# Optimization experiments

Measured on AMD Instinct MI355X. Metric: run time of the kernel, lower is better.

The kernel has to match this reference:

```python
import jax, jax.numpy as jnp
import numpy as np

N_NODES = 50000
N_EDGES = 600000
N_GRAPHS = 64
IN_D, HID, EMB = 5, 128, 64
BN_EPS = 1e-5


def setup_inputs() -> dict:
    key = jax.random.key(0)
    ks = jax.random.split(key, 16)
    x = jax.random.normal(ks[0], (N_NODES, IN_D), dtype=jnp.float32)
    src = jax.random.randint(ks[1], (N_EDGES,), 0, N_NODES, dtype=jnp.int32)
    dst = jax.random.randint(ks[2], (N_EDGES,), 0, N_NODES, dtype=jnp.int32)
    batch = jnp.sort(jax.random.randint(ks[3], (N_NODES,), 0, N_GRAPHS, dtype=jnp.int32))
    def lin(k, fi, fo):
        s = 1.0 / np.sqrt(fi)
        kw, kb = jax.random.split(k)
        return (jax.random.uniform(kw, (fi, fo), jnp.float32, -s, s),
                jax.random.uniform(kb, (fo,), jnp.float32, -s, s))
    W1, b1 = lin(ks[4], IN_D, HID)
    W2, b2 = lin(ks[5], HID, HID)
    W3, b3 = lin(ks[6], HID, HID)
    Wp, bp = lin(ks[7], HID, EMB)
    g1 = 1.0 + 0.1 * jax.random.normal(ks[8], (HID,), jnp.float32)
    g2 = 1.0 + 0.1 * jax.random.normal(ks[9], (HID,), jnp.float32)
    g3 = 1.0 + 0.1 * jax.random.normal(ks[10], (HID,), jnp.float32)
    be1 = 0.1 * jax.random.normal(ks[11], (HID,), jnp.float32)
    be2 = 0.1 * jax.random.normal(ks[12], (HID,), jnp.float32)
    be3 = 0.1 * jax.random.normal(ks[13], (HID,), jnp.float32)
    return dict(x=x, src=src, dst=dst, batch=batch,
                W1=W1, b1=b1, W2=W2, b2=b2, W3=W3, b3=b3,
                g1=g1, be1=be1, g2=g2, be2=be2, g3=g3, be3=be3,
                Wp=Wp, bp=bp)


def reference(x, src, dst, batch, W1, b1, W2, b2, W3, b3,
              g1, be1, g2, be2, g3, be3, Wp, bp):
    n = x.shape[0]
    # GCNConv with self-loops and symmetric normalization (PyG default)
    loop = jnp.arange(n, dtype=src.dtype)
    s = jnp.concatenate([src, loop])
    d = jnp.concatenate([dst, loop])
    deg = jax.ops.segment_sum(jnp.ones_like(d, dtype=x.dtype), d, num_segments=n)
    dinv = jnp.where(deg > 0, jax.lax.rsqrt(deg), 0.0)
    norm = (dinv[s] * dinv[d])[:, None]  # (E+N, 1)

    def gcn(h, W, b):
        hw = h @ W                                   # (N, HID)
        msg = hw[s] * norm                           # gather + scale
        agg = jax.ops.segment_sum(msg, d, num_segments=n)
        return agg + b

    def bn_relu(h, g, be):
        # eval-mode BatchNorm1d with running_mean=0, running_var=1
        return jax.nn.relu(h * (g * jax.lax.rsqrt(jnp.asarray(1.0 + BN_EPS, h.dtype))) + be)

    h = bn_relu(gcn(x, W1, b1), g1, be1)
    h = bn_relu(gcn(h, W2, b2), g2, be2)
    h = bn_relu(gcn(h, W3, b3), g3, be3)

    # global mean pool over graphs
    sums = jax.ops.segment_sum(h, batch, num_segments=N_GRAPHS)
    cnt = jax.ops.segment_sum(jnp.ones((n,), h.dtype), batch, num_segments=N_GRAPHS)
    pooled = sums / jnp.maximum(cnt, 1.0)[:, None]
    return pooled @ Wp + bp
```

## Files before the change

kernel.cpp:

```cpp
#include <hip/hip_runtime.h>
#include <hip/hip_fp16.h>

#define N_NODES 50000
#define N_EDGES 600000
#define N_GRAPHS 64
#define IN_D 5
#define HID 128
#define EMB 64

#define CHUNK 512
#define NCHUNK ((N_NODES + CHUNK - 1) / CHUNK)
#define NREP 16
#define NLOC 4
#define TB 16

typedef _Float16 half8 __attribute__((ext_vector_type(8)));
typedef float float4v __attribute__((ext_vector_type(4)));
typedef float floatx2 __attribute__((ext_vector_type(2)));

__device__ __forceinline__ float ep_w(unsigned pe) {
    return (float)__ushort_as_half((unsigned short)(pe >> 16));
}
__device__ __forceinline__ unsigned ep_s(unsigned pe) { return pe & 0xffffu; }


__global__ __launch_bounds__(256) void k_init(
        int* __restrict__ cnt, float* __restrict__ psum_rep,
        const float* __restrict__ W2, const float* __restrict__ W3,
        _Float16* __restrict__ Wt2, _Float16* __restrict__ Wt3,
        unsigned int* __restrict__ e_pack,
        const float* __restrict__ x, float* __restrict__ xp) {
    int tid = blockIdx.x * blockDim.x + threadIdx.x;
    int nt = gridDim.x * blockDim.x;
    for (int i = tid; i < N_NODES; i += nt) cnt[i] = 0;
    for (int i = tid; i < NREP * N_GRAPHS * HID; i += nt) psum_rep[i] = 0.f;
    if (tid < 8) e_pack[N_EDGES + tid] = 0u;
    for (int i = tid; i < N_NODES * 8; i += nt) {
        int f = i & 7, n = i >> 3;
        xp[i] = (f < IN_D) ? x[n * IN_D + f] : 0.f;
    }
    for (int i = tid; i < 2 * HID * HID; i += nt) {
        int rem = i & (HID * HID - 1);
        int k = rem & 127, f = rem >> 7;
        if (i < HID * HID) Wt2[rem] = (_Float16)W2[k * HID + f];
        else               Wt3[rem] = (_Float16)W3[k * HID + f];
    }
}


__global__ __launch_bounds__(256) void k_count(
        const int* __restrict__ dst, int* __restrict__ cnt) {
    int e = blockIdx.x * blockDim.x + threadIdx.x;
    if (e < N_EDGES) atomicAdd(&cnt[dst[e]], 1);
}


__global__ void k_chunksum(const int* __restrict__ cnt, int* __restrict__ csum,
                           float* __restrict__ dinv) {
    __shared__ int sh[256];
    int b = blockIdx.x, t = threadIdx.x;
    int i0 = b * CHUNK + t, i1 = i0 + 256;
    int v = 0;
    if (i0 < N_NODES) { int c = cnt[i0]; v += c; dinv[i0] = rsqrtf((float)c + 1.0f); }
    if (i1 < N_NODES) { int c = cnt[i1]; v += c; dinv[i1] = rsqrtf((float)c + 1.0f); }
    sh[t] = v; __syncthreads();
    for (int off = 128; off > 0; off >>= 1) {
        if (t < off) sh[t] += sh[t + off];
        __syncthreads();
    }
    if (t == 0) csum[b] = sh[0];
}


__global__ void k_scan(const int* __restrict__ cnt, const int* __restrict__ csum,
                       int* __restrict__ row_start) {
    __shared__ int ws[4];
    int b = blockIdx.x, t = threadIdx.x;
    int lane = t & 63, w = t >> 6;

    int pre = 0;
    for (int j = lane; j < b; j += 64) pre += csum[j];
    #pragma unroll
    for (int off = 32; off > 0; off >>= 1) pre += __shfl_down(pre, off);
    pre = __shfl(pre, 0);

    int base = b * CHUNK;
    int i0 = base + 2 * t, i1 = i0 + 1;
    int c0 = (i0 < N_NODES) ? cnt[i0] : 0;
    int c1 = (i1 < N_NODES) ? cnt[i1] : 0;
    int v = c0 + c1;
    int s = v;
    #pragma unroll
    for (int off = 1; off < 64; off <<= 1) {
        int u = __shfl_up(s, off);
        if (lane >= off) s += u;
    }
    if (lane == 63) ws[w] = s;
    __syncthreads();
    if (t == 0) {
        int r = 0;
        #pragma unroll
        for (int j = 0; j < 4; ++j) { int xx = ws[j]; ws[j] = r; r += xx; }
    }
    __syncthreads();
    int excl = s - v + ws[w] + pre;
    if (i0 < N_NODES) row_start[i0] = excl;
    if (i1 < N_NODES) row_start[i1] = excl + c0;
    if (b == 0 && t == 0) row_start[N_NODES] = N_EDGES;
}


__global__ __launch_bounds__(256) void k_scatter(
        const int* __restrict__ src, const int* __restrict__ dst,
        const float* __restrict__ dinv, const int* __restrict__ row_start,
        int* __restrict__ cnt, unsigned int* __restrict__ e_pack) {
    int e = blockIdx.x * blockDim.x + threadIdx.x;
    if (e >= N_EDGES) return;
    int d = dst[e];
    int pos = row_start[d] + atomicSub(&cnt[d], 1) - 1;
    int s = src[e];
    unsigned hw = (unsigned)__half_as_ushort(__float2half(dinv[s]));
    e_pack[pos] = (hw << 16) | (unsigned)s;
}


__global__ __launch_bounds__(256) void k_agg1(
        const float* __restrict__ xp, const float* __restrict__ dinv,
        const int* __restrict__ row_start, const unsigned int* __restrict__ e_pack,
        const float* __restrict__ W1, const float* __restrict__ b1,
        const float* __restrict__ g1, const float* __restrict__ be1,
        unsigned short* __restrict__ H8u) {
    int t = threadIdx.x;
    int w = t >> 6, lane = t & 63;
    int slot8 = lane >> 3, q8 = lane & 7;
    int nb = blockIdx.x * TB;

    const float rs = rsqrtf(1.0f + 1e-5f);
    int fa = lane * 2, fb = fa + 1;
    float w1a[IN_D], w1b[IN_D];
    #pragma unroll
    for (int k = 0; k < IN_D; ++k) {
        w1a[k] = W1[k * HID + fa];
        w1b[k] = W1[k * HID + fb];
    }
    float b1a = b1[fa], b1b = b1[fb];
    float g1a = g1[fa] * rs, g1b = g1[fb] * rs;
    float e1a = be1[fa], e1b = be1[fb];

    #pragma unroll 1
    for (int i = 0; i < 4; ++i) {
        int n = nb + w * 4 + i;
        int beg = row_start[n], end = row_start[n + 1];
        float acc = 0.f;
        for (int e = beg; e < end; e += 8) {
            unsigned pe = e_pack[e + slot8];
            float fw = (e + slot8 < end) ? ep_w(pe) : 0.f;
            float g = xp[(size_t)ep_s(pe) * 8 + q8];
            acc = fmaf(fw, g, acc);
        }
        acc += __shfl_xor(acc, 8);
        acc += __shfl_xor(acc, 16);
        acc += __shfl_xor(acc, 32);
        float di = dinv[n];
        float av = di * fmaf(di, xp[(size_t)n * 8 + q8], acc);
        float a0 = __shfl(av, 0), a1 = __shfl(av, 1), a2 = __shfl(av, 2),
              a3 = __shfl(av, 3), a4 = __shfl(av, 4);
        float va = b1a, vb = b1b;
        va = fmaf(a0, w1a[0], va); vb = fmaf(a0, w1b[0], vb);
        va = fmaf(a1, w1a[1], va); vb = fmaf(a1, w1b[1], vb);
        va = fmaf(a2, w1a[2], va); vb = fmaf(a2, w1b[2], vb);
        va = fmaf(a3, w1a[3], va); vb = fmaf(a3, w1b[3], vb);
        va = fmaf(a4, w1a[4], va); vb = fmaf(a4, w1b[4], vb);
        va = fmaf(va, g1a, e1a);
        vb = fmaf(vb, g1b, e1b);
        va = va > 0.f ? va : 0.f;
        vb = vb > 0.f ? vb : 0.f;
        int p = __builtin_amdgcn_cvt_pk_fp8_f32(va, vb, 0, false);
        H8u[(size_t)n * 64 + lane] = (unsigned short)(p & 0xffff);
    }
}


__device__ __forceinline__ void agg_node_fp8(
        const unsigned int* __restrict__ H8, const float* __restrict__ dinv,
        const int* __restrict__ row_start, const unsigned int* __restrict__ e_pack,
        int n, int slot8, int q8, _Float16* __restrict__ asrow) {
    float acc[16];
    #pragma unroll
    for (int j = 0; j < 16; ++j) acc[j] = 0.f;
    int beg = row_start[n], end = row_start[n + 1];
    for (int e = beg; e < end; e += 8) {
        unsigned pe = e_pack[e + slot8];
        float fw = (e + slot8 < end) ? ep_w(pe) : 0.f;
        uint4 g = ((const uint4*)(H8 + (size_t)ep_s(pe) * 32))[q8];
        unsigned int gw[4] = {g.x, g.y, g.z, g.w};
        #pragma unroll
        for (int q = 0; q < 4; ++q) {
            floatx2 lo = __builtin_amdgcn_cvt_pk_f32_fp8(gw[q], false);
            floatx2 hi = __builtin_amdgcn_cvt_pk_f32_fp8(gw[q], true);
            acc[4 * q + 0] = fmaf(fw, lo[0], acc[4 * q + 0]);
            acc[4 * q + 1] = fmaf(fw, lo[1], acc[4 * q + 1]);
            acc[4 * q + 2] = fmaf(fw, hi[0], acc[4 * q + 2]);
            acc[4 * q + 3] = fmaf(fw, hi[1], acc[4 * q + 3]);
        }
    }
    #pragma unroll
    for (int j = 0; j < 16; ++j) {
        float a = acc[j];
        a += __shfl_xor(a, 8);
        a += __shfl_xor(a, 16);
        a += __shfl_xor(a, 32);
        acc[j] = a;
    }
    if (slot8 == 0) {
        float di = dinv[n];
        uint4 s = ((const uint4*)(H8 + (size_t)n * 32))[q8];
        unsigned int sw[4] = {s.x, s.y, s.z, s.w};
        float sv[16];
        #pragma unroll
        for (int q = 0; q < 4; ++q) {
            floatx2 lo = __builtin_amdgcn_cvt_pk_f32_fp8(sw[q], false);
            floatx2 hi = __builtin_amdgcn_cvt_pk_f32_fp8(sw[q], true);
            sv[4 * q + 0] = lo[0]; sv[4 * q + 1] = lo[1];
            sv[4 * q + 2] = hi[0]; sv[4 * q + 3] = hi[1];
        }
        half8 o0, o1;
        #pragma unroll
        for (int j = 0; j < 8; ++j)
            o0[j] = (_Float16)(di * fmaf(di, sv[j], acc[j]));
        #pragma unroll
        for (int j = 0; j < 8; ++j)
            o1[j] = (_Float16)(di * fmaf(di, sv[j + 8], acc[j + 8]));
        *(half8*)(asrow + q8 * 16) = o0;
        *(half8*)(asrow + q8 * 16 + 8) = o1;
    }
}


__global__ __launch_bounds__(256) void k_fuse2(
        const unsigned int* __restrict__ Hin, const float* __restrict__ dinv,
        const int* __restrict__ row_start, const unsigned int* __restrict__ e_pack,
        const _Float16* __restrict__ Wt,
        const float* __restrict__ bb, const float* __restrict__ gg,
        const float* __restrict__ bee, unsigned char* __restrict__ out8) {
    __shared__ __align__(16) _Float16 As[TB][136];
    int t = threadIdx.x;
    int w = t >> 6, lane = t & 63;
    int slot8 = lane >> 3, q8 = lane & 7;
    int nb = blockIdx.x * TB;

    #pragma unroll 1
    for (int i = 0; i < 4; ++i)
        agg_node_fp8(Hin, dinv, row_start, e_pack,
                     nb + w * 4 + i, slot8, q8, &As[w * 4 + i][0]);
    __syncthreads();

    int quad = lane >> 4, r16 = lane & 15;
    half8 a[4];
    #pragma unroll
    for (int kb = 0; kb < 4; ++kb)
        a[kb] = *(const half8*)&As[r16][(kb * 4 + quad) * 8];
    const float rs = rsqrtf(1.0f + 1e-5f);
    #pragma unroll
    for (int fi = 0; fi < 2; ++fi) {
        int f = (w * 2 + fi) * 16 + r16;
        const half8* Brow = (const half8*)(Wt + (size_t)f * 128);
        float4v acc = {0.f, 0.f, 0.f, 0.f};
        #pragma unroll
        for (int kb = 0; kb < 4; ++kb)
            acc = __builtin_amdgcn_mfma_f32_16x16x32_f16(a[kb], Brow[kb * 4 + quad],
                                                         acc, 0, 0, 0);
        float b0 = bb[f], gf = gg[f] * rs, e0 = bee[f];
        #pragma unroll
        for (int rr = 0; rr < 4; ++rr) {
            float v = fmaf(acc[rr] + b0, gf, e0);
            v = v > 0.f ? v : 0.f;
            int p = __builtin_amdgcn_cvt_pk_fp8_f32(v, 0.f, 0, false);
            out8[(size_t)(nb + quad * 4 + rr) * 128 + f] = (unsigned char)(p & 0xff);
        }
    }
}


__global__ __launch_bounds__(256) void k_fuse3(
        const unsigned int* __restrict__ Hin, const float* __restrict__ dinv,
        const int* __restrict__ row_start, const unsigned int* __restrict__ e_pack,
        const _Float16* __restrict__ Wt,
        const float* __restrict__ bb, const float* __restrict__ gg,
        const float* __restrict__ bee, const int* __restrict__ batch,
        float* __restrict__ psum_rep) {
    __shared__ __align__(16) _Float16 As[TB][136];
    __shared__ float sh_pool[NLOC][HID];
    int t = threadIdx.x;
    int w = t >> 6, lane = t & 63;
    int slot8 = lane >> 3, q8 = lane & 7;
    int blk = (int)blockIdx.x;
    int nb = blk * TB;

    for (int i = t; i < NLOC * HID; i += 256) ((float*)sh_pool)[i] = 0.f;
    __syncthreads();

    #pragma unroll 1
    for (int i = 0; i < 4; ++i)
        agg_node_fp8(Hin, dinv, row_start, e_pack,
                     nb + w * 4 + i, slot8, q8, &As[w * 4 + i][0]);

    int quad = lane >> 4, r16 = lane & 15;
    int g0 = batch[nb];
    int gi4[4];
    #pragma unroll
    for (int rr = 0; rr < 4; ++rr) gi4[rr] = batch[nb + quad * 4 + rr];
    __syncthreads();

    half8 a[4];
    #pragma unroll
    for (int kb = 0; kb < 4; ++kb)
        a[kb] = *(const half8*)&As[r16][(kb * 4 + quad) * 8];
    float* rep = psum_rep + (size_t)(blk & (NREP - 1)) * N_GRAPHS * HID;
    const float rs = rsqrtf(1.0f + 1e-5f);
    #pragma unroll
    for (int fi = 0; fi < 2; ++fi) {
        int f = (w * 2 + fi) * 16 + r16;
        const half8* Brow = (const half8*)(Wt + (size_t)f * 128);
        float4v acc = {0.f, 0.f, 0.f, 0.f};
        #pragma unroll
        for (int kb = 0; kb < 4; ++kb)
            acc = __builtin_amdgcn_mfma_f32_16x16x32_f16(a[kb], Brow[kb * 4 + quad],
                                                         acc, 0, 0, 0);
        float b0 = bb[f], gf = gg[f] * rs, e0 = bee[f];
        float partial = 0.f;
        int cur = -1;
        #pragma unroll
        for (int rr = 0; rr < 4; ++rr) {
            float v = fmaf(acc[rr] + b0, gf, e0);
            v = v > 0.f ? v : 0.f;
            int gi = gi4[rr];
            if (gi != cur) {
                if (cur >= 0) {
                    int idx = cur - g0;
                    if (idx < NLOC) atomicAdd(&sh_pool[idx][f], partial);
                    else            atomicAdd(&rep[cur * HID + f], partial);
                }
                partial = 0.f; cur = gi;
            }
            partial += v;
        }
        if (cur >= 0) {
            int idx = cur - g0;
            if (idx < NLOC) atomicAdd(&sh_pool[idx][f], partial);
            else            atomicAdd(&rep[cur * HID + f], partial);
        }
    }
    __syncthreads();
    for (int i = t; i < NLOC * HID; i += 256) {
        int idx = i >> 7, ff = i & 127;
        float v = sh_pool[idx][ff];
        int g = g0 + idx;
        if (v != 0.f && g < N_GRAPHS) atomicAdd(&rep[g * HID + ff], v);
    }
}


__device__ __forceinline__ int lower_bound_batch(const int* __restrict__ batch, int val) {
    int lo = 0, hi = N_NODES;
    while (lo < hi) {
        int mid = (lo + hi) >> 1;
        if (batch[mid] < val) lo = mid + 1;
        else hi = mid;
    }
    return lo;
}

__global__ void k_final(const float* __restrict__ psum_rep, const int* __restrict__ batch,
                        const float* __restrict__ Wp, const float* __restrict__ bp,
                        float* __restrict__ out) {
    __shared__ float s_p[HID];
    int gi = blockIdx.x, e = threadIdx.x;
    for (int f = e; f < HID; f += EMB) {
        float v = 0.f;
        #pragma unroll
        for (int r = 0; r < NREP; ++r)
            v += psum_rep[(size_t)r * N_GRAPHS * HID + gi * HID + f];
        s_p[f] = v;
    }
    int lane = e & 63;
    int r = 0;
    if (lane < 2) r = lower_bound_batch(batch, gi + lane);
    int c0 = __shfl(r, 0), c1 = __shfl(r, 1);
    float inv = 1.0f / fmaxf((float)(c1 - c0), 1.0f);
    __syncthreads();
    float acc = bp[e];
    #pragma unroll 8
    for (int f = 0; f < HID; ++f)
        acc = fmaf(s_p[f] * inv, Wp[f * EMB + e], acc);
    out[gi * EMB + e] = acc;
}


extern "C" void kernel_launch(void* const* d_in, const int* in_sizes, int n_in,
                              void* d_out, int out_size, void* d_ws, size_t ws_size,
                              hipStream_t stream) {
    const float* x   = (const float*)d_in[0];
    const int*   src = (const int*)d_in[1];
    const int*   dst = (const int*)d_in[2];
    const int* batch = (const int*)d_in[3];
    const float* W1 = (const float*)d_in[4];
    const float* b1 = (const float*)d_in[5];
    const float* W2 = (const float*)d_in[6];
    const float* b2 = (const float*)d_in[7];
    const float* W3 = (const float*)d_in[8];
    const float* b3 = (const float*)d_in[9];
    const float* g1 = (const float*)d_in[10];
    const float* be1 = (const float*)d_in[11];
    const float* g2 = (const float*)d_in[12];
    const float* be2 = (const float*)d_in[13];
    const float* g3 = (const float*)d_in[14];
    const float* be3 = (const float*)d_in[15];
    const float* Wp = (const float*)d_in[16];
    const float* bp = (const float*)d_in[17];
    float* out = (float*)d_out;

    char* ws = (char*)d_ws;
    size_t o = 0;
    auto alloc = [&](size_t bytes) {
        void* pp = ws + o;
        o += bytes;
        o = (o + 255) & ~255ull;
        return pp;
    };
    int*      cnt       = (int*)alloc(N_NODES * 4);
    int*      row_start = (int*)alloc((N_NODES + 1) * 4);
    int*      csum      = (int*)alloc(NCHUNK * 4);
    float*    dinv      = (float*)alloc(N_NODES * 4);
    unsigned int* e_pack = (unsigned int*)alloc((size_t)(N_EDGES + 8) * 4);
    _Float16* Wt2       = (_Float16*)alloc(HID * HID * 2);
    _Float16* Wt3       = (_Float16*)alloc(HID * HID * 2);
    float*    xp        = (float*)alloc((size_t)N_NODES * 8 * 4);
    unsigned int* H8a   = (unsigned int*)alloc((size_t)N_NODES * HID);
    unsigned int* H8b   = (unsigned int*)alloc((size_t)N_NODES * HID);
    float*    psum_rep  = (float*)alloc((size_t)NREP * N_GRAPHS * HID * 4);

    k_init<<<512, 256, 0, stream>>>(cnt, psum_rep, W2, W3, Wt2, Wt3, e_pack, x, xp);
    k_count<<<(N_EDGES + 255) / 256, 256, 0, stream>>>(dst, cnt);
    k_chunksum<<<NCHUNK, 256, 0, stream>>>(cnt, csum, dinv);
    k_scan<<<NCHUNK, 256, 0, stream>>>(cnt, csum, row_start);
    k_scatter<<<(N_EDGES + 255) / 256, 256, 0, stream>>>(src, dst, dinv, row_start,
                                                         cnt, e_pack);
    k_agg1<<<N_NODES / TB, 256, 0, stream>>>(xp, dinv, row_start, e_pack,
                                             W1, b1, g1, be1, (unsigned short*)H8a);
    k_fuse2<<<N_NODES / TB, 256, 0, stream>>>(H8a, dinv, row_start, e_pack, Wt2,
                                              b2, g2, be2, (unsigned char*)H8b);
    k_fuse3<<<N_NODES / TB, 256, 0, stream>>>(H8b, dinv, row_start, e_pack, Wt3,
                                              b3, g3, be3, batch, psum_rep);
    k_final<<<N_GRAPHS, EMB, 0, stream>>>(psum_rep, batch, Wp, bp, out);
}
```

Before: 270.7 us.

## Interleave edge gathers for node pairs and fold setup work into count kernel

New measurement: 262.5 us. 3.0% less time.

```diff
diff --git a/kernel.cpp b/kernel.cpp
--- a/kernel.cpp
+++ b/kernel.cpp
@@ -24,17 +24,24 @@
 __device__ __forceinline__ unsigned ep_s(unsigned pe) { return pe & 0xffffu; }
 
 
-__global__ __launch_bounds__(256) void k_init(
-        int* __restrict__ cnt, float* __restrict__ psum_rep,
+__global__ __launch_bounds__(256) void k_init(int* __restrict__ cnt) {
+    int tid = blockIdx.x * blockDim.x + threadIdx.x;
+    if (tid < N_NODES) cnt[tid] = 0;
+}
+
+
+__global__ __launch_bounds__(256) void k_count(
+        const int* __restrict__ dst, int* __restrict__ cnt,
+        float* __restrict__ psum_rep,
         const float* __restrict__ W2, const float* __restrict__ W3,
         _Float16* __restrict__ Wt2, _Float16* __restrict__ Wt3,
         unsigned int* __restrict__ e_pack,
         const float* __restrict__ x, float* __restrict__ xp) {
     int tid = blockIdx.x * blockDim.x + threadIdx.x;
     int nt = gridDim.x * blockDim.x;
-    for (int i = tid; i < N_NODES; i += nt) cnt[i] = 0;
+    if (tid < N_EDGES) atomicAdd(&cnt[dst[tid]], 1);
+    if (tid < 8) e_pack[N_EDGES + tid] = 0u;
     for (int i = tid; i < NREP * N_GRAPHS * HID; i += nt) psum_rep[i] = 0.f;
-    if (tid < 8) e_pack[N_EDGES + tid] = 0u;
     for (int i = tid; i < N_NODES * 8; i += nt) {
         int f = i & 7, n = i >> 3;
         xp[i] = (f < IN_D) ? x[n * IN_D + f] : 0.f;
@@ -45,13 +52,6 @@
         if (i < HID * HID) Wt2[rem] = (_Float16)W2[k * HID + f];
         else               Wt3[rem] = (_Float16)W3[k * HID + f];
     }
-}
-
-
-__global__ __launch_bounds__(256) void k_count(
-        const int* __restrict__ dst, int* __restrict__ cnt) {
-    int e = blockIdx.x * blockDim.x + threadIdx.x;
-    if (e < N_EDGES) atomicAdd(&cnt[dst[e]], 1);
 }
 
 
@@ -148,91 +148,149 @@
     float e1a = be1[fa], e1b = be1[fb];
 
     #pragma unroll 1
-    for (int i = 0; i < 4; ++i) {
-        int n = nb + w * 4 + i;
-        int beg = row_start[n], end = row_start[n + 1];
-        float acc = 0.f;
-        for (int e = beg; e < end; e += 8) {
-            unsigned pe = e_pack[e + slot8];
-            float fw = (e + slot8 < end) ? ep_w(pe) : 0.f;
-            float g = xp[(size_t)ep_s(pe) * 8 + q8];
-            acc = fmaf(fw, g, acc);
-        }
-        acc += __shfl_xor(acc, 8);
-        acc += __shfl_xor(acc, 16);
-        acc += __shfl_xor(acc, 32);
-        float di = dinv[n];
-        float av = di * fmaf(di, xp[(size_t)n * 8 + q8], acc);
-        float a0 = __shfl(av, 0), a1 = __shfl(av, 1), a2 = __shfl(av, 2),
-              a3 = __shfl(av, 3), a4 = __shfl(av, 4);
-        float va = b1a, vb = b1b;
-        va = fmaf(a0, w1a[0], va); vb = fmaf(a0, w1b[0], vb);
-        va = fmaf(a1, w1a[1], va); vb = fmaf(a1, w1b[1], vb);
-        va = fmaf(a2, w1a[2], va); vb = fmaf(a2, w1b[2], vb);
-        va = fmaf(a3, w1a[3], va); vb = fmaf(a3, w1b[3], vb);
-        va = fmaf(a4, w1a[4], va); vb = fmaf(a4, w1b[4], vb);
-        va = fmaf(va, g1a, e1a);
-        vb = fmaf(vb, g1b, e1b);
-        va = va > 0.f ? va : 0.f;
-        vb = vb > 0.f ? vb : 0.f;
-        int p = __builtin_amdgcn_cvt_pk_fp8_f32(va, vb, 0, false);
-        H8u[(size_t)n * 64 + lane] = (unsigned short)(p & 0xffff);
-    }
-}
-
-
-__device__ __forceinline__ void agg_node_fp8(
+    for (int i = 0; i < 2; ++i) {
+        int n0 = nb + w * 4 + i * 2;
+        int beg0 = row_start[n0], end0 = row_start[n0 + 1], end1 = row_start[n0 + 2];
+        float acc0 = 0.f, acc1 = 0.f;
+        int e0 = beg0, e1 = end0;
+        while (e0 < end0 && e1 < end1) {
+            unsigned pe0 = e_pack[e0 + slot8];
+            unsigned pe1 = e_pack[e1 + slot8];
+            float fw0 = (e0 + slot8 < end0) ? ep_w(pe0) : 0.f;
+            float fw1 = (e1 + slot8 < end1) ? ep_w(pe1) : 0.f;
+            float v0 = xp[(size_t)ep_s(pe0) * 8 + q8];
+            float v1 = xp[(size_t)ep_s(pe1) * 8 + q8];
+            acc0 = fmaf(fw0, v0, acc0);
+            acc1 = fmaf(fw1, v1, acc1);
+            e0 += 8; e1 += 8;
+        }
+        while (e0 < end0) {
+            unsigned pe0 = e_pack[e0 + slot8];
+            float fw0 = (e0 + slot8 < end0) ? ep_w(pe0) : 0.f;
+            acc0 = fmaf(fw0, xp[(size_t)ep_s(pe0) * 8 + q8], acc0);
+            e0 += 8;
+        }
+        while (e1 < end1) {
+            unsigned pe1 = e_pack[e1 + slot8];
+            float fw1 = (e1 + slot8 < end1) ? ep_w(pe1) : 0.f;
+            acc1 = fmaf(fw1, xp[(size_t)ep_s(pe1) * 8 + q8], acc1);
+            e1 += 8;
+        }
+        #pragma unroll
+        for (int off = 8; off < 64; off <<= 1) {
+            acc0 += __shfl_xor(acc0, off);
+            acc1 += __shfl_xor(acc1, off);
+        }
+        #pragma unroll
+        for (int p2 = 0; p2 < 2; ++p2) {
+            int n = n0 + p2;
+            float accs = p2 ? acc1 : acc0;
+            float di = dinv[n];
+            float av = di * fmaf(di, xp[(size_t)n * 8 + q8], accs);
+            float a0 = __shfl(av, 0), a1 = __shfl(av, 1), a2 = __shfl(av, 2),
+                  a3 = __shfl(av, 3), a4 = __shfl(av, 4);
+            float va = b1a, vb = b1b;
+            va = fmaf(a0, w1a[0], va); vb = fmaf(a0, w1b[0], vb);
+            va = fmaf(a1, w1a[1], va); vb = fmaf(a1, w1b[1], vb);
+            va = fmaf(a2, w1a[2], va); vb = fmaf(a2, w1b[2], vb);
+            va = fmaf(a3, w1a[3], va); vb = fmaf(a3, w1b[3], vb);
+            va = fmaf(a4, w1a[4], va); vb = fmaf(a4, w1b[4], vb);
+            va = fmaf(va, g1a, e1a);
+            vb = fmaf(vb, g1b, e1b);
+            va = va > 0.f ? va : 0.f;
+            vb = vb > 0.f ? vb : 0.f;
+            int p = __builtin_amdgcn_cvt_pk_fp8_f32(va, vb, 0, false);
+            H8u[(size_t)n * 64 + lane] = (unsigned short)(p & 0xffff);
+        }
+    }
+}
+
+
+__device__ __forceinline__ void acc_row_fp8(float* __restrict__ acc, float fw, uint4 g) {
+    unsigned int gw[4] = {g.x, g.y, g.z, g.w};
+    #pragma unroll
+    for (int q = 0; q < 4; ++q) {
+        floatx2 lo = __builtin_amdgcn_cvt_pk_f32_fp8(gw[q], false);
+        floatx2 hi = __builtin_amdgcn_cvt_pk_f32_fp8(gw[q], true);
+        acc[4 * q + 0] = fmaf(fw, lo[0], acc[4 * q + 0]);
+        acc[4 * q + 1] = fmaf(fw, lo[1], acc[4 * q + 1]);
+        acc[4 * q + 2] = fmaf(fw, hi[0], acc[4 * q + 2]);
+        acc[4 * q + 3] = fmaf(fw, hi[1], acc[4 * q + 3]);
+    }
+}
+
+__device__ __forceinline__ void agg_pair_fp8(
         const unsigned int* __restrict__ H8, const float* __restrict__ dinv,
         const int* __restrict__ row_start, const unsigned int* __restrict__ e_pack,
-        int n, int slot8, int q8, _Float16* __restrict__ asrow) {
-    float acc[16];
-    #pragma unroll
-    for (int j = 0; j < 16; ++j) acc[j] = 0.f;
-    int beg = row_start[n], end = row_start[n + 1];
-    for (int e = beg; e < end; e += 8) {
-        unsigned pe = e_pack[e + slot8];
-        float fw = (e + slot8 < end) ? ep_w(pe) : 0.f;
-        uint4 g = ((const uint4*)(H8 + (size_t)ep_s(pe) * 32))[q8];
-        unsigned int gw[4] = {g.x, g.y, g.z, g.w};
+        int n0, int slot8, int q8,
+        _Float16* __restrict__ row0, _Float16* __restrict__ row1) {
+    float acc0[16], acc1[16];
+    #pragma unroll
+    for (int j = 0; j < 16; ++j) { acc0[j] = 0.f; acc1[j] = 0.f; }
+    int beg0 = row_start[n0], end0 = row_start[n0 + 1], end1 = row_start[n0 + 2];
+    int e0 = beg0, e1 = end0;
+    while (e0 < end0 && e1 < end1) {
+        unsigned pe0 = e_pack[e0 + slot8];
+        unsigned pe1 = e_pack[e1 + slot8];
+        float fw0 = (e0 + slot8 < end0) ? ep_w(pe0) : 0.f;
+        float fw1 = (e1 + slot8 < end1) ? ep_w(pe1) : 0.f;
+        uint4 g0 = ((const uint4*)(H8 + (size_t)ep_s(pe0) * 32))[q8];
+        uint4 g1 = ((const uint4*)(H8 + (size_t)ep_s(pe1) * 32))[q8];
+        acc_row_fp8(acc0, fw0, g0);
+        acc_row_fp8(acc1, fw1, g1);
+        e0 += 8; e1 += 8;
+    }
+    while (e0 < end0) {
+        unsigned pe0 = e_pack[e0 + slot8];
+        float fw0 = (e0 + slot8 < end0) ? ep_w(pe0) : 0.f;
+        uint4 g0 = ((const uint4*)(H8 + (size_t)ep_s(pe0) * 32))[q8];
+        acc_row_fp8(acc0, fw0, g0);
+        e0 += 8;
+    }
+    while (e1 < end1) {
+        unsigned pe1 = e_pack[e1 + slot8];
+        float fw1 = (e1 + slot8 < end1) ? ep_w(pe1) : 0.f;
+        uint4 g1 = ((const uint4*)(H8 + (size_t)ep_s(pe1) * 32))[q8];
+        acc_row_fp8(acc1, fw1, g1);
+        e1 += 8;
+    }
+    #pragma unroll
+    for (int j = 0; j < 16; ++j) {
+        float a = acc0[j];
+        a += __shfl_xor(a, 8); a += __shfl_xor(a, 16); a += __shfl_xor(a, 32);
+        acc0[j] = a;
+        float b = acc1[j];
+        b += __shfl_xor(b, 8); b += __shfl_xor(b, 16); b += __shfl_xor(b, 32);
+        acc1[j] = b;
+    }
+    if (slot8 == 0) {
+        float di0 = dinv[n0], di1 = dinv[n0 + 1];
+        uint4 s0 = ((const uint4*)(H8 + (size_t)n0 * 32))[q8];
+        uint4 s1 = ((const uint4*)(H8 + (size_t)(n0 + 1) * 32))[q8];
+        unsigned int sw0[4] = {s0.x, s0.y, s0.z, s0.w};
+        unsigned int sw1[4] = {s1.x, s1.y, s1.z, s1.w};
+        half8 o0a, o0b, o1a, o1b;
         #pragma unroll
         for (int q = 0; q < 4; ++q) {
-            floatx2 lo = __builtin_amdgcn_cvt_pk_f32_fp8(gw[q], false);
-            floatx2 hi = __builtin_amdgcn_cvt_pk_f32_fp8(gw[q], true);
-            acc[4 * q + 0] = fmaf(fw, lo[0], acc[4 * q + 0]);
-            acc[4 * q + 1] = fmaf(fw, lo[1], acc[4 * q + 1]);
-            acc[4 * q + 2] = fmaf(fw, hi[0], acc[4 * q + 2]);
-            acc[4 * q + 3] = fmaf(fw, hi[1], acc[4 * q + 3]);
-        }
-    }
-    #pragma unroll
-    for (int j = 0; j < 16; ++j) {
-        float a = acc[j];
-        a += __shfl_xor(a, 8);
-        a += __shfl_xor(a, 16);
-        a += __shfl_xor(a, 32);
-        acc[j] = a;
-    }
-    if (slot8 == 0) {
-        float di = dinv[n];
-        uint4 s = ((const uint4*)(H8 + (size_t)n * 32))[q8];
-        unsigned int sw[4] = {s.x, s.y, s.z, s.w};
-        float sv[16];
-        #pragma unroll
-        for (int q = 0; q < 4; ++q) {
-            floatx2 lo = __builtin_amdgcn_cvt_pk_f32_fp8(sw[q], false);
-            floatx2 hi = __builtin_amdgcn_cvt_pk_f32_fp8(sw[q], true);
-            sv[4 * q + 0] = lo[0]; sv[4 * q + 1] = lo[1];
-            sv[4 * q + 2] = hi[0]; sv[4 * q + 3] = hi[1];
-        }
-        half8 o0, o1;
-        #pragma unroll
-        for (int j = 0; j < 8; ++j)
-            o0[j] = (_Float16)(di * fmaf(di, sv[j], acc[j]));
-        #pragma unroll
-        for (int j = 0; j < 8; ++j)
-            o1[j] = (_Float16)(di * fmaf(di, sv[j + 8], acc[j + 8]));
-        *(half8*)(asrow + q8 * 16) = o0;
-        *(half8*)(asrow + q8 * 16 + 8) = o1;
+            floatx2 lo0 = __builtin_amdgcn_cvt_pk_f32_fp8(sw0[q], false);
+            floatx2 hi0 = __builtin_amdgcn_cvt_pk_f32_fp8(sw0[q], true);
+            floatx2 lo1 = __builtin_amdgcn_cvt_pk_f32_fp8(sw1[q], false);
+            floatx2 hi1 = __builtin_amdgcn_cvt_pk_f32_fp8(sw1[q], true);
+            int j = 4 * q;
+            float f0[4] = {lo0[0], lo0[1], hi0[0], hi0[1]};
+            float f1[4] = {lo1[0], lo1[1], hi1[0], hi1[1]};
+            #pragma unroll
+            for (int u = 0; u < 4; ++u) {
+                float r0 = di0 * fmaf(di0, f0[u], acc0[j + u]);
+                float r1 = di1 * fmaf(di1, f1[u], acc1[j + u]);
+                if (j + u < 8) { o0a[j + u] = (_Float16)r0; o1a[j + u] = (_Float16)r1; }
+                else           { o0b[j + u - 8] = (_Float16)r0; o1b[j + u - 8] = (_Float16)r1; }
+            }
+        }
+        *(half8*)(row0 + q8 * 16)     = o0a;
+        *(half8*)(row0 + q8 * 16 + 8) = o0b;
+        *(half8*)(row1 + q8 * 16)     = o1a;
+        *(half8*)(row1 + q8 * 16 + 8) = o1b;
     }
 }
 
@@ -250,9 +308,9 @@
     int nb = blockIdx.x * TB;
 
     #pragma unroll 1
-    for (int i = 0; i < 4; ++i)
-        agg_node_fp8(Hin, dinv, row_start, e_pack,
-                     nb + w * 4 + i, slot8, q8, &As[w * 4 + i][0]);
+    for (int i = 0; i < 2; ++i)
+        agg_pair_fp8(Hin, dinv, row_start, e_pack, nb + w * 4 + i * 2,
+                     slot8, q8, &As[w * 4 + i * 2][0], &As[w * 4 + i * 2 + 1][0]);
     __syncthreads();
 
     int quad = lane >> 4, r16 = lane & 15;
@@ -301,9 +359,9 @@
     __syncthreads();
 
     #pragma unroll 1
-    for (int i = 0; i < 4; ++i)
-        agg_node_fp8(Hin, dinv, row_start, e_pack,
-                     nb + w * 4 + i, slot8, q8, &As[w * 4 + i][0]);
+    for (int i = 0; i < 2; ++i)
+        agg_pair_fp8(Hin, dinv, row_start, e_pack, nb + w * 4 + i * 2,
+                     slot8, q8, &As[w * 4 + i * 2][0], &As[w * 4 + i * 2 + 1][0]);
 
     int quad = lane >> 4, r16 = lane & 15;
     int g0 = batch[nb];
@@ -440,8 +498,9 @@
     unsigned int* H8b   = (unsigned int*)alloc((size_t)N_NODES * HID);
     float*    psum_rep  = (float*)alloc((size_t)NREP * N_GRAPHS * HID * 4);
 
-    k_init<<<512, 256, 0, stream>>>(cnt, psum_rep, W2, W3, Wt2, Wt3, e_pack, x, xp);
-    k_count<<<(N_EDGES + 255) / 256, 256, 0, stream>>>(dst, cnt);
+    k_init<<<(N_NODES + 255) / 256, 256, 0, stream>>>(cnt);
+    k_count<<<(N_EDGES + 255) / 256, 256, 0, stream>>>(dst, cnt, psum_rep,
+                                                       W2, W3, Wt2, Wt3, e_pack, x, xp);
     k_chunksum<<<NCHUNK, 256, 0, stream>>>(cnt, csum, dinv);
     k_scan<<<NCHUNK, 256, 0, stream>>>(cnt, csum, row_start);
     k_scatter<<<(N_EDGES + 255) / 256, 256, 0, stream>>>(src, dst, dinv, row_start,
```
